# Optimization experiments

Measured on AMD Instinct MI355X. Metric: run time of the kernel, lower is better.

## Reference

```python
import jax, jax.numpy as jnp
import numpy as np

N, E = 50000, 800000
IN, HID, OUT = 128, 256, 40
EPS = 1e-5


def setup_inputs() -> dict:
    key = jax.random.key(0)
    ks = jax.random.split(key, 16)
    def glorot(k, shape):
        lim = float(np.sqrt(6.0 / (shape[0] + shape[1])))
        return jax.random.uniform(k, shape, jnp.float32, -lim, lim)
    return {
        "x": jax.random.normal(ks[0], (N, IN), jnp.float32),
        "edge_index": jax.random.randint(ks[1], (2, E), 0, N, jnp.int64),
        "W1": glorot(ks[2], (IN, HID)),  "b1": jnp.zeros((HID,), jnp.float32),
        "g1": jnp.ones((HID,), jnp.float32), "be1": jnp.zeros((HID,), jnp.float32),
        "W2": glorot(ks[3], (HID, HID)), "b2": jnp.zeros((HID,), jnp.float32),
        "g2": jnp.ones((HID,), jnp.float32), "be2": jnp.zeros((HID,), jnp.float32),
        "W3": glorot(ks[4], (HID, OUT)), "b3": jnp.zeros((OUT,), jnp.float32),
        "Wl": glorot(ks[5], (OUT, OUT)), "bl": jnp.zeros((OUT,), jnp.float32),
    }


def _gcn_conv(h, src, dst, norm, W, b, n):
    # PyG GCNConv: transform, then normalized scatter-add over edges (+self-loops)
    m = h @ W                                     # [N, d_out]
    msg = m[src] * norm[:, None]                  # gather + edge scale
    out = jax.ops.segment_sum(msg, dst, num_segments=n)
    return out + b


def _bn(h, g, b):
    # BatchNorm1d (training-mode batch stats, biased variance)
    mu = jnp.mean(h, axis=0)
    var = jnp.var(h, axis=0)
    return (h - mu) * jax.lax.rsqrt(var + EPS) * g + b


def reference(x, edge_index, W1, b1, g1, be1, W2, b2, g2, be2, W3, b3, Wl, bl):
    n = x.shape[0]
    loops = jnp.arange(n, dtype=edge_index.dtype)
    src = jnp.concatenate([edge_index[0], loops])
    dst = jnp.concatenate([edge_index[1], loops])
    deg = jax.ops.segment_sum(jnp.ones(src.shape[0], x.dtype), dst, num_segments=n)
    dinv = jnp.where(deg > 0, jax.lax.rsqrt(deg), 0.0)
    norm = dinv[src] * dinv[dst]

    h = jax.nn.relu(_bn(_gcn_conv(x, src, dst, norm, W1, b1, n), g1, be1))
    h = jax.nn.relu(_bn(_gcn_conv(h, src, dst, norm, W2, b2, n), g2, be2))
    h = _gcn_conv(h, src, dst, norm, W3, b3, n)
    h = h @ Wl + bl
    return jax.nn.log_softmax(h, axis=1)
```

## Files before the change

### kernel.cpp

```cpp
#include <hip/hip_runtime.h>
#include <hip/hip_bf16.h>
#include <math.h>

#define IN_DIM 128
#define HID 256
#define OUT_DIM 40
#define OUT_PAD 64
#define CAP 64
#define EPS 1e-5f

typedef __attribute__((ext_vector_type(8))) short short8;
typedef __attribute__((ext_vector_type(4))) float floatx4;

__device__ __forceinline__ float b2f(unsigned short u) {
    union { unsigned int i; float f; } c; c.i = ((unsigned int)u) << 16; return c.f;
}
__device__ __forceinline__ unsigned short f2b(float f) {
    union { float f; unsigned int i; } c; c.f = f;
    unsigned int r = c.i + 0x7FFF + ((c.i >> 16) & 1);
    return (unsigned short)(r >> 16);
}

union U8 { uint4 u; unsigned short s[8]; };
union F8 { short8 v; unsigned short s[8]; uint4 u; };


__global__ void fill1_k(const int* __restrict__ src, const int* __restrict__ dst,
                        int* __restrict__ cnt, unsigned short* __restrict__ col2, int E,
                        const float* __restrict__ W1, const float* __restrict__ W2,
                        const float* __restrict__ W3, const float* __restrict__ Wl,
                        const float* __restrict__ b3, const float* __restrict__ bl,
                        unsigned short* __restrict__ W1t, unsigned short* __restrict__ W2t,
                        unsigned short* __restrict__ W3lt, float* __restrict__ bias2,
                        float* __restrict__ stats1, float* __restrict__ stats2,
                        const float* __restrict__ x, unsigned short* __restrict__ xb,
                        int N) {
    if (blockIdx.x < 2048) {
        for (int e = blockIdx.x * 256 + threadIdx.x; e < E; e += 2048 * 256) {
            int d = dst[e];
            int p = atomicAdd(&cnt[d], 1);
            if (p < CAP) col2[(size_t)d * CAP + p] = (unsigned short)src[e];
        }
    } else if (blockIdx.x < 2560) {
        const int n1 = 256 * 128, n2 = 256 * 256;
        int j = (blockIdx.x - 2048) * 256 + threadIdx.x;
        if (j < n1) {
            int n = j >> 7, k = j & 127;
            W1t[j] = f2b(W1[k * 256 + n]);
        } else if (j < n1 + n2) {
            int j2 = j - n1;
            int n = j2 >> 8, k = j2 & 255;
            W2t[j2] = f2b(W2[k * 256 + n]);
        } else {
            int j3 = j - n1 - n2;
            int n = j3 >> 8, k = j3 & 255;
            float acc = 0.f;
            if (n < OUT_DIM) {
                for (int q = 0; q < OUT_DIM; ++q)
                    acc += W3[k * OUT_DIM + q] * Wl[q * OUT_DIM + n];
            }
            W3lt[j3] = (n < OUT_DIM) ? f2b(acc) : 0;
            if (j3 < OUT_DIM) {
                float b = bl[j3];
                for (int q = 0; q < OUT_DIM; ++q) b += b3[q] * Wl[q * OUT_DIM + j3];
                bias2[j3] = b;
            }
        }
    } else if (blockIdx.x == 2560) {
        int t = threadIdx.x;
        stats1[t] = 0.f; stats1[256 + t] = 0.f;
        stats2[t] = 0.f; stats2[256 + t] = 0.f;
    } else {
        size_t nx = (size_t)N * 32;
        size_t nbk = gridDim.x - 2561;
        for (size_t i = (size_t)(blockIdx.x - 2561) * 256 + threadIdx.x; i < nx;
             i += nbk * 256) {
            float4 v = ((const float4*)x)[i];
            ushort4 o;
            o.x = f2b(v.x); o.y = f2b(v.y); o.z = f2b(v.z); o.w = f2b(v.w);
            ((ushort4*)xb)[i] = o;
        }
    }
}


template <int NW, bool BN, bool STATS>
__global__ __launch_bounds__(NW * 64) void gemm_t(const unsigned short* __restrict__ A,
                                                  const unsigned short* __restrict__ Bt,
                                                  unsigned short* __restrict__ C,
                                                  const int* __restrict__ cnt,
                                                  const float* __restrict__ bias,
                                                  const float* __restrict__ bnstats,
                                                  const float* __restrict__ g,
                                                  const float* __restrict__ be,
                                                  float* __restrict__ gstats,
                                                  float invN,
                                                  int M, int Nc, int K, int ldc) {
    __shared__ unsigned short As[NW * 16][40];
    __shared__ unsigned short Bs[64][40];
    __shared__ float s_sc[BN ? HID : 1], s_sh[BN ? HID : 1];
    __shared__ float ls1[STATS ? 64 : 1], ls2[STATS ? 64 : 1];
    int tid = threadIdx.x;
    if (BN) {
        for (int t = tid; t < K; t += NW * 64) {
            float mu = bnstats[t] * invN;
            float var = bnstats[HID + t] * invN - mu * mu;
            float sc = g[t] * rsqrtf(var + EPS);
            s_sc[t] = sc;
            s_sh[t] = be[t] - mu * sc;
        }
    }
    if (STATS && tid < 64) { ls1[tid] = 0.f; ls2[tid] = 0.f; }
    __syncthreads();

    int wave = tid >> 6, lane = tid & 63;
    int r16 = lane & 15, quad = lane >> 4;
    int row0 = blockIdx.y * (NW * 16), col0 = blockIdx.x * 64;

    floatx4 acc[4] = {};

    int sr = tid >> 2, sko = (tid & 3) * 8;
    for (int k0 = 0; k0 < K; k0 += 32) {
        {
            int ar = min(row0 + sr, M - 1);
            U8 ra;
            ra.u = *(const uint4*)&A[(size_t)ar * K + k0 + sko];
            if (BN) {
#pragma unroll
                for (int j = 0; j < 8; ++j) {
                    int kk = k0 + sko + j;
                    float f = b2f(ra.s[j]) * s_sc[kk] + s_sh[kk];
                    ra.s[j] = f2b(fmaxf(f, 0.f));
                }
            }
            *(uint4*)&As[sr][sko] = ra.u;
        }
#pragma unroll
        for (int j = 0; j < 4 / NW; ++j) {
            int idx = tid + j * NW * 64;
            int br = idx >> 2, bko = (idx & 3) * 8;
            *(uint4*)&Bs[br][bko] = *(const uint4*)&Bt[(size_t)(col0 + br) * K + k0 + bko];
        }
        __syncthreads();
        F8 a, b[4];
        a.u = *(const uint4*)&As[wave * 16 + r16][quad * 8];
#pragma unroll
        for (int nt = 0; nt < 4; ++nt)
            b[nt].u = *(const uint4*)&Bs[nt * 16 + r16][quad * 8];
#pragma unroll
        for (int nt = 0; nt < 4; ++nt)
            acc[nt] = __builtin_amdgcn_mfma_f32_16x16x32_bf16(a.v, b[nt].v, acc[nt], 0, 0, 0);
        __syncthreads();
    }

    float s1[4] = {0.f, 0.f, 0.f, 0.f}, s2[4] = {0.f, 0.f, 0.f, 0.f};
#pragma unroll
    for (int r = 0; r < 4; ++r) {
        int row = row0 + wave * 16 + quad * 4 + r;
        if (row >= M) continue;
        float dv = cnt ? rsqrtf((float)(cnt[row] + 1)) : 1.f;
#pragma unroll
        for (int nt = 0; nt < 4; ++nt) {
            int colg = col0 + nt * 16 + r16;
            if (colg < Nc) {
                float v = acc[nt][r] * dv + (bias ? bias[colg] : 0.f);
                C[(size_t)row * ldc + colg] = f2b(v);
                if (STATS) { s1[nt] += v; s2[nt] += v * v; }
            }
        }
    }
    if (STATS) {
#pragma unroll
        for (int nt = 0; nt < 4; ++nt) {
            s1[nt] += __shfl_xor(s1[nt], 16); s1[nt] += __shfl_xor(s1[nt], 32);
            s2[nt] += __shfl_xor(s2[nt], 16); s2[nt] += __shfl_xor(s2[nt], 32);
            if (quad == 0) {
                atomicAdd(&ls1[nt * 16 + r16], s1[nt]);
                atomicAdd(&ls2[nt * 16 + r16], s2[nt]);
            }
        }
        __syncthreads();
        if (tid < 64) {
            int cg = col0 + tid;
            atomicAdd(&gstats[cg], ls1[tid]);
            atomicAdd(&gstats[HID + cg], ls2[tid]);
        }
    }
}


__global__ __launch_bounds__(256, 8) void agg_x(const unsigned short* __restrict__ m,
                                                const unsigned short* __restrict__ col2,
                                                const int* __restrict__ cnt,
                                                unsigned short* __restrict__ out,
                                                int N) {
    int v = blockIdx.x * 4 + (threadIdx.x >> 6);
    if (v >= N) return;
    int lane = threadIdx.x & 63;
    int q = lane >> 4;
    int c0 = (lane & 15) * 8;
    int cv = cnt[v];
    float dv = rsqrtf((float)(cv + 1));
    const unsigned short* col = col2 + (size_t)v * CAP;
    int end = min(cv, CAP);
    float a[8] = {};
    {
        U8 r; r.u = *(const uint4*)&m[(size_t)v * IN_DIM + c0];
#pragma unroll
        for (int k = 0; k < 8; ++k) a[k] = b2f(r.s[k]) * dv;
    }
    if (q != 0) { a[0]=a[1]=a[2]=a[3]=a[4]=a[5]=a[6]=a[7]=0.f; }
    int e = 0;
    for (; e + 8 <= end; e += 8) {
        int idx[2];
#pragma unroll
        for (int j = 0; j < 2; ++j) idx[j] = col[e + 4 * j + q];
        float ds[2];
#pragma unroll
        for (int j = 0; j < 2; ++j) ds[j] = rsqrtf((float)(cnt[idx[j]] + 1));
        U8 rr[2];
#pragma unroll
        for (int j = 0; j < 2; ++j)
            rr[j].u = *(const uint4*)&m[(size_t)idx[j] * IN_DIM + c0];
#pragma unroll
        for (int j = 0; j < 2; ++j)
#pragma unroll
            for (int k = 0; k < 8; ++k) a[k] += b2f(rr[j].s[k]) * ds[j];
    }
    for (; e < end; e += 4) {
        int t = e + q;
        if (t < end) {
            int s = col[t];
            float ds = rsqrtf((float)(cnt[s] + 1));
            U8 r; r.u = *(const uint4*)&m[(size_t)s * IN_DIM + c0];
#pragma unroll
            for (int k = 0; k < 8; ++k) a[k] += b2f(r.s[k]) * ds;
        }
    }
#pragma unroll
    for (int k = 0; k < 8; ++k) {
        a[k] += __shfl_xor(a[k], 16);
        a[k] += __shfl_xor(a[k], 32);
    }
    if (q == 0) {
        U8 o;
#pragma unroll
        for (int k = 0; k < 8; ++k) o.s[k] = f2b(a[k] * dv);
        *(uint4*)&out[(size_t)v * IN_DIM + c0] = o.u;
    }
}

__global__ __launch_bounds__(256, 8) void agg_h(const unsigned short* __restrict__ m,
                                                const unsigned short* __restrict__ col2,
                                                const int* __restrict__ cnt,
                                                const float* __restrict__ bias,
                                                unsigned short* __restrict__ out,
                                                int N) {
    int v = blockIdx.x * 4 + (threadIdx.x >> 6);
    if (v >= N) return;
    int lane = threadIdx.x & 63;
    int half = lane >> 5;
    int c0 = (lane & 31) * 8;
    int cv = cnt[v];
    float dv = rsqrtf((float)(cv + 1));
    const unsigned short* col = col2 + (size_t)v * CAP;
    int end = min(cv, CAP);
    float a[8] = {};
    if (half == 0) {
        U8 r; r.u = *(const uint4*)&m[(size_t)v * HID + c0];
#pragma unroll
        for (int k = 0; k < 8; ++k) a[k] = b2f(r.s[k]);
    }
    int e = 0;
    for (; e + 8 <= end; e += 8) {
        int idx[4];
#pragma unroll
        for (int j = 0; j < 4; ++j) idx[j] = col[e + 2 * j + half];
        U8 rr[4];
#pragma unroll
        for (int j = 0; j < 4; ++j)
            rr[j].u = *(const uint4*)&m[(size_t)idx[j] * HID + c0];
#pragma unroll
        for (int j = 0; j < 4; ++j)
#pragma unroll
            for (int k = 0; k < 8; ++k) a[k] += b2f(rr[j].s[k]);
    }
    for (; e < end; e += 2) {
        int t = e + half;
        if (t < end) {
            U8 r; r.u = *(const uint4*)&m[(size_t)col[t] * HID + c0];
#pragma unroll
            for (int k = 0; k < 8; ++k) a[k] += b2f(r.s[k]);
        }
    }
#pragma unroll
    for (int k = 0; k < 8; ++k) a[k] += __shfl_xor(a[k], 32);
    if (half == 0) {
        U8 o;
#pragma unroll
        for (int k = 0; k < 8; ++k) o.s[k] = f2b(a[k] * dv + bias[c0 + k]);
        *(uint4*)&out[(size_t)v * HID + c0] = o.u;
    }
}

__global__ __launch_bounds__(256, 8) void agg_o_ls(const unsigned short* __restrict__ m,
                                                   const unsigned short* __restrict__ col2,
                                                   const int* __restrict__ cnt,
                                                   const float* __restrict__ bias2,
                                                   float* __restrict__ out,
                                                   int N) {
    int v = blockIdx.x * 4 + (threadIdx.x >> 6);
    if (v >= N) return;
    int lane = threadIdx.x & 63;
    int slot = lane >> 3;
    int li = lane & 7;
    int c0 = li * 8;
    int cv = cnt[v];
    float dv = rsqrtf((float)(cv + 1));
    const unsigned short* col = col2 + (size_t)v * CAP;
    int end = min(cv, CAP);
    float a[8] = {};
    if (slot == 0) {
        U8 r; r.u = *(const uint4*)&m[(size_t)v * OUT_PAD + c0];
#pragma unroll
        for (int k = 0; k < 8; ++k) a[k] = b2f(r.s[k]);
    }
    int e = 0;
    for (; e + 16 <= end; e += 16) {
        int idx[2];
        idx[0] = col[e + slot];
        idx[1] = col[e + 8 + slot];
        U8 rr[2];
#pragma unroll
        for (int j = 0; j < 2; ++j)
            rr[j].u = *(const uint4*)&m[(size_t)idx[j] * OUT_PAD + c0];
#pragma unroll
        for (int j = 0; j < 2; ++j)
#pragma unroll
            for (int k = 0; k < 8; ++k) a[k] += b2f(rr[j].s[k]);
    }
    for (; e < end; e += 8) {
        int t = e + slot;
        if (t < end) {
            U8 r; r.u = *(const uint4*)&m[(size_t)col[t] * OUT_PAD + c0];
#pragma unroll
            for (int k = 0; k < 8; ++k) a[k] += b2f(r.s[k]);
        }
    }
#pragma unroll
    for (int k = 0; k < 8; ++k) {
        a[k] += __shfl_xor(a[k], 8);
        a[k] += __shfl_xor(a[k], 16);
        a[k] += __shfl_xor(a[k], 32);
    }
    bool valid = (li < 5);
    float mx = -INFINITY;
#pragma unroll
    for (int k = 0; k < 8; ++k) {
        float val = valid ? (a[k] * dv + bias2[c0 + k]) : -INFINITY;
        a[k] = val;
        mx = fmaxf(mx, val);
    }
    mx = fmaxf(mx, __shfl_xor(mx, 1));
    mx = fmaxf(mx, __shfl_xor(mx, 2));
    mx = fmaxf(mx, __shfl_xor(mx, 4));
    float s = 0.f;
    if (valid) {
#pragma unroll
        for (int k = 0; k < 8; ++k) s += expf(a[k] - mx);
    }
    s += __shfl_xor(s, 1);
    s += __shfl_xor(s, 2);
    s += __shfl_xor(s, 4);
    float ls = mx + logf(s);
    if (slot == 0 && valid) {
        float4 o0, o1;
        o0.x = a[0] - ls; o0.y = a[1] - ls; o0.z = a[2] - ls; o0.w = a[3] - ls;
        o1.x = a[4] - ls; o1.y = a[5] - ls; o1.z = a[6] - ls; o1.w = a[7] - ls;
        float* p = &out[(size_t)v * OUT_DIM + c0];
        *(float4*)p = o0;
        *(float4*)(p + 4) = o1;
    }
}


__global__ __launch_bounds__(256) void bn_stats(const unsigned short* __restrict__ h,
                                                float* __restrict__ stats, int N) {
    __shared__ float ls[8][2][256];
    int t = threadIdx.x;
    int walker = t >> 5;
    int c0 = (t & 31) * 8;
    int r0 = blockIdx.x * 128;
    int rend = min(r0 + 128, N);
    float s1[8] = {}, s2[8] = {};
    for (int r = r0 + walker; r < rend; r += 8) {
        U8 x; x.u = *(const uint4*)&h[(size_t)r * HID + c0];
#pragma unroll
        for (int k = 0; k < 8; ++k) {
            float v = b2f(x.s[k]);
            s1[k] += v; s2[k] += v * v;
        }
    }
#pragma unroll
    for (int k = 0; k < 8; ++k) {
        ls[walker][0][c0 + k] = s1[k];
        ls[walker][1][c0 + k] = s2[k];
    }
    __syncthreads();
    float a1 = 0.f, a2 = 0.f;
#pragma unroll
    for (int w = 0; w < 8; ++w) { a1 += ls[w][0][t]; a2 += ls[w][1][t]; }
    atomicAdd(&stats[t], a1);
    atomicAdd(&stats[HID + t], a2);
}


extern "C" void kernel_launch(void* const* d_in, const int* in_sizes, int n_in,
                              void* d_out, int out_size, void* d_ws, size_t ws_size,
                              hipStream_t stream) {
    const float* x   = (const float*)d_in[0];
    const int*  eidx = (const int*)d_in[1];
    const float* W1 = (const float*)d_in[2];
    const float* b1 = (const float*)d_in[3];
    const float* g1 = (const float*)d_in[4];
    const float* be1 = (const float*)d_in[5];
    const float* W2 = (const float*)d_in[6];
    const float* b2 = (const float*)d_in[7];
    const float* g2 = (const float*)d_in[8];
    const float* be2 = (const float*)d_in[9];
    const float* W3 = (const float*)d_in[10];
    const float* b3 = (const float*)d_in[11];
    const float* Wl = (const float*)d_in[12];
    const float* bl = (const float*)d_in[13];
    float* out = (float*)d_out;

    const int N = in_sizes[0] / IN_DIM;
    const int E = in_sizes[1] / 2;
    const int* src = eidx;
    const int* dst = eidx + E;

    size_t off = 0;
    char* ws = (char*)d_ws;
    auto carve = [&](size_t bytes) -> void* {
        void* p = ws + off;
        off += (bytes + 255) & ~(size_t)255;
        return p;
    };
    int*   cnt  = (int*)carve((size_t)N * 4);
    float* stats1 = (float*)carve((size_t)2 * HID * 4);
    float* stats2 = (float*)carve((size_t)2 * HID * 4);
    unsigned short* col2 = (unsigned short*)carve((size_t)N * CAP * 2);
    unsigned short* xb   = (unsigned short*)carve((size_t)N * IN_DIM * 2);
    unsigned short* axb  = (unsigned short*)carve((size_t)N * IN_DIM * 2);
    unsigned short* W1t  = (unsigned short*)carve((size_t)256 * IN_DIM * 2);
    unsigned short* W2t  = (unsigned short*)carve((size_t)256 * HID * 2);
    unsigned short* W3lt = (unsigned short*)carve((size_t)128 * HID * 2);
    float* bias2 = (float*)carve((size_t)OUT_DIM * 4);
    unsigned short* mbuf = (unsigned short*)carve((size_t)N * HID * 2);
    unsigned short* hbuf = (unsigned short*)carve((size_t)N * HID * 2);

    hipMemsetAsync(cnt, 0, (size_t)N * 4, stream);
    int xconvBlocks = (int)(((size_t)N * 32 + 255) / 256);
    fill1_k<<<2561 + xconvBlocks, 256, 0, stream>>>(src, dst, cnt, col2, E,
                                                    W1, W2, W3, Wl, b3, bl,
                                                    W1t, W2t, W3lt, bias2,
                                                    stats1, stats2, x, xb, N);

    int nodeBlocks = (N + 3) / 4;
    float invN = 1.f / (float)N;
    int mb64 = (N + 63) / 64;
    int mb32 = (N + 31) / 32;

    agg_x<<<nodeBlocks, 256, 0, stream>>>(xb, col2, cnt, axb, N);
    gemm_t<4, false, true><<<dim3(4, mb64), 256, 0, stream>>>(axb, W1t, hbuf,
                                                              nullptr, b1,
                                                              nullptr, nullptr, nullptr,
                                                              stats1, invN,
                                                              N, HID, IN_DIM, HID);

    gemm_t<4, true, false><<<dim3(4, mb64), 256, 0, stream>>>(hbuf, W2t, mbuf,
                                                              cnt, nullptr,
                                                              stats1, g1, be1,
                                                              nullptr, invN,
                                                              N, HID, HID, HID);
    agg_h<<<nodeBlocks, 256, 0, stream>>>(mbuf, col2, cnt, b2, hbuf, N);
    bn_stats<<<(N + 127) / 128, 256, 0, stream>>>(hbuf, stats2, N);

    gemm_t<2, true, false><<<dim3(1, mb32), 128, 0, stream>>>(hbuf, W3lt, mbuf,
                                                              cnt, nullptr,
                                                              stats2, g2, be2,
                                                              nullptr, invN,
                                                              N, OUT_PAD, HID, OUT_PAD);
    agg_o_ls<<<nodeBlocks, 256, 0, stream>>>(mbuf, col2, cnt, bias2, out, N);
}
```

Baseline: 366.2 us.

## Widen GEMM tiles to 128 columns and 64-deep K steps

```diff
diff --git a/kernel.cpp b/kernel.cpp
--- a/kernel.cpp
+++ b/kernel.cpp
@@ -84,25 +84,28 @@
 }
 
 
-template <int NW, bool BN, bool STATS>
-__global__ __launch_bounds__(NW * 64) void gemm_t(const unsigned short* __restrict__ A,
-                                                  const unsigned short* __restrict__ Bt,
-                                                  unsigned short* __restrict__ C,
-                                                  const int* __restrict__ cnt,
-                                                  const float* __restrict__ bias,
-                                                  const float* __restrict__ bnstats,
-                                                  const float* __restrict__ g,
-                                                  const float* __restrict__ be,
-                                                  float* __restrict__ gstats,
-                                                  float invN,
-                                                  int M, int Nc, int K, int ldc) {
-    __shared__ unsigned short As[NW * 16][40];
-    __shared__ unsigned short Bs[64][40];
+template <int ROWS, bool BN, bool STATS>
+__global__ __launch_bounds__(ROWS * 4) void gemm_t(const unsigned short* __restrict__ A,
+                                                   const unsigned short* __restrict__ Bt,
+                                                   unsigned short* __restrict__ C,
+                                                   const int* __restrict__ cnt,
+                                                   const float* __restrict__ bias,
+                                                   const float* __restrict__ bnstats,
+                                                   const float* __restrict__ g,
+                                                   const float* __restrict__ be,
+                                                   float* __restrict__ gstats,
+                                                   float invN,
+                                                   int M, int Nc, int K, int ldc) {
+    constexpr int COLS = ROWS * 2;
+    constexpr int NT = COLS / 16;
+    constexpr int T = ROWS * 4;
+    __shared__ unsigned short As[ROWS][72];
+    __shared__ unsigned short Bs[COLS][72];
     __shared__ float s_sc[BN ? HID : 1], s_sh[BN ? HID : 1];
-    __shared__ float ls1[STATS ? 64 : 1], ls2[STATS ? 64 : 1];
+    __shared__ float ls1[STATS ? COLS : 1], ls2[STATS ? COLS : 1];
     int tid = threadIdx.x;
     if (BN) {
-        for (int t = tid; t < K; t += NW * 64) {
+        for (int t = tid; t < K; t += T) {
             float mu = bnstats[t] * invN;
             float var = bnstats[HID + t] * invN - mu * mu;
             float sc = g[t] * rsqrtf(var + EPS);
@@ -110,57 +113,64 @@
             s_sh[t] = be[t] - mu * sc;
         }
     }
-    if (STATS && tid < 64) { ls1[tid] = 0.f; ls2[tid] = 0.f; }
+    if (STATS && tid < COLS) { ls1[tid] = 0.f; ls2[tid] = 0.f; }
     __syncthreads();
 
     int wave = tid >> 6, lane = tid & 63;
     int r16 = lane & 15, quad = lane >> 4;
-    int row0 = blockIdx.y * (NW * 16), col0 = blockIdx.x * 64;
-
-    floatx4 acc[4] = {};
-
-    int sr = tid >> 2, sko = (tid & 3) * 8;
-    for (int k0 = 0; k0 < K; k0 += 32) {
-        {
-            int ar = min(row0 + sr, M - 1);
+    int row0 = blockIdx.y * ROWS, col0 = blockIdx.x * COLS;
+
+    floatx4 acc[NT] = {};
+
+    for (int k0 = 0; k0 < K; k0 += 64) {
+#pragma unroll
+        for (int i = 0; i < 2; ++i) {
+            int ci = tid + i * T;
+            int r = ci >> 3, ko = (ci & 7) * 8;
+            int ar = min(row0 + r, M - 1);
             U8 ra;
-            ra.u = *(const uint4*)&A[(size_t)ar * K + k0 + sko];
+            ra.u = *(const uint4*)&A[(size_t)ar * K + k0 + ko];
             if (BN) {
 #pragma unroll
                 for (int j = 0; j < 8; ++j) {
-                    int kk = k0 + sko + j;
+                    int kk = k0 + ko + j;
                     float f = b2f(ra.s[j]) * s_sc[kk] + s_sh[kk];
                     ra.s[j] = f2b(fmaxf(f, 0.f));
                 }
             }
-            *(uint4*)&As[sr][sko] = ra.u;
-        }
-#pragma unroll
-        for (int j = 0; j < 4 / NW; ++j) {
-            int idx = tid + j * NW * 64;
-            int br = idx >> 2, bko = (idx & 3) * 8;
-            *(uint4*)&Bs[br][bko] = *(const uint4*)&Bt[(size_t)(col0 + br) * K + k0 + bko];
+            *(uint4*)&As[r][ko] = ra.u;
+        }
+#pragma unroll
+        for (int i = 0; i < 4; ++i) {
+            int ci = tid + i * T;
+            int r = ci >> 3, ko = (ci & 7) * 8;
+            *(uint4*)&Bs[r][ko] = *(const uint4*)&Bt[(size_t)(col0 + r) * K + k0 + ko];
         }
         __syncthreads();
-        F8 a, b[4];
-        a.u = *(const uint4*)&As[wave * 16 + r16][quad * 8];
-#pragma unroll
-        for (int nt = 0; nt < 4; ++nt)
-            b[nt].u = *(const uint4*)&Bs[nt * 16 + r16][quad * 8];
-#pragma unroll
-        for (int nt = 0; nt < 4; ++nt)
-            acc[nt] = __builtin_amdgcn_mfma_f32_16x16x32_bf16(a.v, b[nt].v, acc[nt], 0, 0, 0);
+#pragma unroll
+        for (int ks = 0; ks < 64; ks += 32) {
+            F8 a;
+            a.u = *(const uint4*)&As[wave * 16 + r16][ks + quad * 8];
+#pragma unroll
+            for (int nt = 0; nt < NT; ++nt) {
+                F8 b;
+                b.u = *(const uint4*)&Bs[nt * 16 + r16][ks + quad * 8];
+                acc[nt] = __builtin_amdgcn_mfma_f32_16x16x32_bf16(a.v, b.v, acc[nt], 0, 0, 0);
+            }
+        }
         __syncthreads();
     }
 
-    float s1[4] = {0.f, 0.f, 0.f, 0.f}, s2[4] = {0.f, 0.f, 0.f, 0.f};
+    float s1[NT], s2[NT];
+#pragma unroll
+    for (int nt = 0; nt < NT; ++nt) { s1[nt] = 0.f; s2[nt] = 0.f; }
 #pragma unroll
     for (int r = 0; r < 4; ++r) {
         int row = row0 + wave * 16 + quad * 4 + r;
         if (row >= M) continue;
         float dv = cnt ? rsqrtf((float)(cnt[row] + 1)) : 1.f;
 #pragma unroll
-        for (int nt = 0; nt < 4; ++nt) {
+        for (int nt = 0; nt < NT; ++nt) {
             int colg = col0 + nt * 16 + r16;
             if (colg < Nc) {
                 float v = acc[nt][r] * dv + (bias ? bias[colg] : 0.f);
@@ -171,7 +181,7 @@
     }
     if (STATS) {
 #pragma unroll
-        for (int nt = 0; nt < 4; ++nt) {
+        for (int nt = 0; nt < NT; ++nt) {
             s1[nt] += __shfl_xor(s1[nt], 16); s1[nt] += __shfl_xor(s1[nt], 32);
             s2[nt] += __shfl_xor(s2[nt], 16); s2[nt] += __shfl_xor(s2[nt], 32);
             if (quad == 0) {
@@ -180,7 +190,7 @@
             }
         }
         __syncthreads();
-        if (tid < 64) {
+        if (tid < COLS) {
             int cg = col0 + tid;
             atomicAdd(&gstats[cg], ls1[tid]);
             atomicAdd(&gstats[HID + cg], ls2[tid]);
@@ -472,24 +482,24 @@
     int mb32 = (N + 31) / 32;
 
     agg_x<<<nodeBlocks, 256, 0, stream>>>(xb, col2, cnt, axb, N);
-    gemm_t<4, false, true><<<dim3(4, mb64), 256, 0, stream>>>(axb, W1t, hbuf,
-                                                              nullptr, b1,
-                                                              nullptr, nullptr, nullptr,
-                                                              stats1, invN,
-                                                              N, HID, IN_DIM, HID);
-
-    gemm_t<4, true, false><<<dim3(4, mb64), 256, 0, stream>>>(hbuf, W2t, mbuf,
-                                                              cnt, nullptr,
-                                                              stats1, g1, be1,
-                                                              nullptr, invN,
-                                                              N, HID, HID, HID);
+    gemm_t<64, false, true><<<dim3(2, mb64), 256, 0, stream>>>(axb, W1t, hbuf,
+                                                               nullptr, b1,
+                                                               nullptr, nullptr, nullptr,
+                                                               stats1, invN,
+                                                               N, HID, IN_DIM, HID);
+
+    gemm_t<64, true, false><<<dim3(2, mb64), 256, 0, stream>>>(hbuf, W2t, mbuf,
+                                                               cnt, nullptr,
+                                                               stats1, g1, be1,
+                                                               nullptr, invN,
+                                                               N, HID, HID, HID);
     agg_h<<<nodeBlocks, 256, 0, stream>>>(mbuf, col2, cnt, b2, hbuf, N);
     bn_stats<<<(N + 127) / 128, 256, 0, stream>>>(hbuf, stats2, N);
 
-    gemm_t<2, true, false><<<dim3(1, mb32), 128, 0, stream>>>(hbuf, W3lt, mbuf,
-                                                              cnt, nullptr,
-                                                              stats2, g2, be2,
-                                                              nullptr, invN,
-                                                              N, OUT_PAD, HID, OUT_PAD);
+    gemm_t<32, true, false><<<dim3(1, mb32), 128, 0, stream>>>(hbuf, W3lt, mbuf,
+                                                               cnt, nullptr,
+                                                               stats2, g2, be2,
+                                                               nullptr, invN,
+                                                               N, OUT_PAD, HID, OUT_PAD);
     agg_o_ls<<<nodeBlocks, 256, 0, stream>>>(mbuf, col2, cnt, bias2, out, N);
 }
```

Result: slower. 378.8 us (+3.4%).
